# Kernel tuning notes

Hardware: AMD Instinct MI355X
Metric: run time of the kernel (lower is better)

The kernel has to match this reference:

```python
import jax, jax.numpy as jnp
import numpy as np

S, N, F, E, H = 64, 1000, 64, 128, 2  # seq_len, nodes/graph, node_dim, emb_dim, heads
DEG = 8
C = E // H  # per-head channels


def setup_inputs() -> dict:
    key = jax.random.key(0)
    ks = jax.random.split(key, 16)
    Ntot = S * N
    Eg = N * DEG
    src = jax.random.randint(ks[0], (S, Eg), 0, N)
    dst = jax.random.randint(ks[1], (S, Eg), 0, N)
    off = (jnp.arange(S) * N)[:, None]
    edge_index = jnp.stack([(src + off).reshape(-1), (dst + off).reshape(-1)]).astype(jnp.int32)
    nfm = jax.random.normal(ks[2], (Ntot, F), jnp.float32)
    reachable = jax.random.uniform(ks[3], (S, N)) > 0.2
    reachable = reachable.at[:, 0].set(True)  # ensure each row has a reachable node
    h0 = jnp.zeros((N, E), jnp.float32)
    c0 = jnp.zeros((N, E), jnp.float32)

    def lin(k, i, o):
        return (jax.random.normal(k, (i, o), jnp.float32) / np.sqrt(i)).astype(jnp.float32)

    return dict(
        nfm=nfm, edge_index=edge_index, reachable=reachable, h0=h0, c0=c0,
        gat_W1=lin(ks[4], F, E), gat_b1=jnp.zeros((E,), jnp.float32),
        gat_att1=(jax.random.normal(ks[5], (H, C), jnp.float32) / np.sqrt(C)).astype(jnp.float32),
        gat_bias1=jnp.zeros((E,), jnp.float32),
        gat_W=(jax.random.normal(ks[6], (4, E, E), jnp.float32) / np.sqrt(E)).astype(jnp.float32),
        gat_b=jnp.zeros((4, E), jnp.float32),
        gat_att=(jax.random.normal(ks[7], (4, H, C), jnp.float32) / np.sqrt(C)).astype(jnp.float32),
        gat_bias=jnp.zeros((4, E), jnp.float32),
        lstm_Wih=(jax.random.normal(ks[8], (4 * E, E), jnp.float32) / np.sqrt(E)).astype(jnp.float32),
        lstm_Whh=(jax.random.normal(ks[9], (4 * E, E), jnp.float32) / np.sqrt(E)).astype(jnp.float32),
        lstm_bih=jnp.zeros((4 * E,), jnp.float32), lstm_bhh=jnp.zeros((4 * E,), jnp.float32),
        th6_W=lin(ks[10], E, E), th6_b=jnp.zeros((E,), jnp.float32),
        th7_W=lin(ks[11], E, E), th7_b=jnp.zeros((E,), jnp.float32),
        th5_W=lin(ks[12], 2 * E, 1), th5_b=jnp.zeros((1,), jnp.float32),
    )


def _gat_layer(x, src, dst, W, b, att, bias, Ntot):
    # GATv2Conv, share_weights=True: x_l == x_r = lin(x)
    Hh, Ch = att.shape
    xl = (x @ W + b).reshape(-1, Hh, Ch)                 # [Ntot,H,C]
    e = jax.nn.leaky_relu(xl[src] + xl[dst], 0.2)        # [Etot,H,C]
    logit = jnp.einsum('ehc,hc->eh', e, att)             # [Etot,H]
    m = jax.ops.segment_max(logit, dst, num_segments=Ntot)
    a = jnp.exp(logit - m[dst])                          # segment-stable softmax
    denom = jax.ops.segment_sum(a, dst, num_segments=Ntot)
    alpha = a / denom[dst]
    out = jax.ops.segment_sum(xl[src] * alpha[:, :, None], dst, num_segments=Ntot)
    return out.reshape(-1, Hh * Ch) + bias               # concat heads + bias


def _forward(nfm, edge_index, reachable, h0, c0, gat_W1, gat_b1, gat_att1, gat_bias1,
             gat_W, gat_b, gat_att, gat_bias, lstm_Wih, lstm_Whh, lstm_bih, lstm_bhh,
             th6_W, th6_b, th7_W, th7_b, th5_W, th5_b):
    Ntot = nfm.shape[0]
    loops = jnp.arange(Ntot, dtype=edge_index.dtype)     # add_self_loops=True
    src = jnp.concatenate([edge_index[0], loops])
    dst = jnp.concatenate([edge_index[1], loops])

    x = jax.nn.relu(_gat_layer(nfm, src, dst, gat_W1, gat_b1, gat_att1, gat_bias1, Ntot))
    for i in range(4):  # layers 2..5; no activation after last
        x = _gat_layer(x, src, dst, gat_W[i], gat_b[i], gat_att[i], gat_bias[i], Ntot)
        if i < 3:
            x = jax.nn.relu(x)

    mu = x.reshape(S, N, E)                              # [seq, batch(=nodes), emb]

    def step(carry, xt):
        h, c = carry
        g = xt @ lstm_Wih.T + lstm_bih + h @ lstm_Whh.T + lstm_bhh
        i_, f_, gg, o_ = jnp.split(g, 4, axis=-1)        # torch gate order i,f,g,o
        c = jax.nn.sigmoid(f_) * c + jax.nn.sigmoid(i_) * jnp.tanh(gg)
        h = jax.nn.sigmoid(o_) * jnp.tanh(c)
        return (h, c), h

    (hT, cT), mu = jax.lax.scan(step, (h0, c0), mu)      # mu: [S,N,E]

    meanpool = mu.mean(axis=1, keepdims=True)            # [S,1,E]
    gs = meanpool @ th6_W + th6_b
    la = mu @ th7_W + th7_b
    rep = jax.nn.relu(jnp.concatenate([jnp.broadcast_to(gs, la.shape), la], axis=-1))
    logits = (rep @ th5_W)[..., 0] + th5_b               # [S,N]
    logits = jnp.where(reachable, logits, -jnp.inf)
    prob = jax.nn.softmax(logits, axis=1)
    return prob, hT, cT


def reference(nfm, edge_index, reachable, h0, c0, gat_W1, gat_b1, gat_att1, gat_bias1,
              gat_W, gat_b, gat_att, gat_bias, lstm_Wih, lstm_Whh, lstm_bih, lstm_bhh,
              th6_W, th6_b, th7_W, th7_b, th5_W, th5_b):
    return _forward(nfm, edge_index, reachable, h0, c0, gat_W1, gat_b1, gat_att1, gat_bias1,
                    gat_W, gat_b, gat_att, gat_bias, lstm_Wih, lstm_Whh, lstm_bih, lstm_bhh,
                    th6_W, th6_b, th7_W, th7_b, th5_W, th5_b)
```

## Files before the change

### kernel.cpp

```cpp
#include <hip/hip_runtime.h>
#include <hip/hip_bf16.h>

#define SQ   64
#define NN   1000
#define NT   64000
#define EE   128
#define EG   512000
#define ET   576000

#define WS_XA      0ull
#define WS_XB      33000000ull
#define WS_ROWPTR  66000000ull
#define WS_CURSOR  66300000ull
#define WS_SRCS    66600000ull
#define WS_INCL    69000000ull
#define WS_BSUM    69300000ull
#define WS_BOFF    69302048ull
#define WS_MODE    69304096ull
#define WS_WQA     70000000ull
#define WS_WQB     70262144ull
#define WS_AS      70600000ull
#define WS_LOGIT2  70700000ull
#define WS2_XC     33000000ull
#define WS2_BFRAG  164100000ull
#define WS2_GHI    164300000ull
#define WS2_GLO    164650000ull
#define WS2_B512   165000000ull
#define WS2_MODE   165010000ull
#define WS2_AS     165020000ull
#define WS2_LOGIT2 165100000ull
#define WS2_NEED   165360000ull
#define G_W1    0
#define G_WL    8192
#define G_PROJ  73728
#define G_W7    139264

typedef __attribute__((ext_vector_type(8))) short short8;
typedef __attribute__((ext_vector_type(4))) float f32x4;

__device__ __forceinline__ float rdlane(float v, int l) {
    return __int_as_float(__builtin_amdgcn_readlane(__float_as_int(v), l));
}
__device__ __forceinline__ float sigm(float x) { return 1.0f / (1.0f + __expf(-x)); }
__device__ __forceinline__ float tanh_f(float x) {
    x = fminf(fmaxf(x, -30.0f), 30.0f);
    float e = __expf(2.0f * x);
    return (e - 1.0f) / (e + 1.0f);
}
__device__ __forceinline__ float tanh2(float x) {
    return 2.0f / (1.0f + __expf(-2.0f * x)) - 1.0f;
}
__device__ __forceinline__ ushort f2bf(float x) {
    unsigned u = __float_as_uint(x);
    unsigned r = (u + 0x7FFFu + ((u >> 16) & 1u)) >> 16;
    return (ushort)r;
}
__device__ __forceinline__ float bf2f(ushort h) {
    return __uint_as_float(((unsigned)h) << 16);
}

__global__ void detect_mode_k(const unsigned char* __restrict__ p, int* __restrict__ mode) {
    __shared__ int f0, f3;
    const int t = threadIdx.x;
    if (t == 0) { f0 = 0; f3 = 0; }
    __syncthreads();
    int l0 = 0, l3 = 0;
    for (int i = t; i < 16000; i += 256) {
        if (p[4 * i])     l0 = 1;
        if (p[4 * i + 3]) l3 = 1;
    }
    if (l0) atomicOr(&f0, 1);
    if (l3) atomicOr(&f3, 1);
    __syncthreads();
    if (t == 0) {
        int m;
        if (f0 && f3)      m = 1;
        else if (f0)       m = 0;
        else               m = 2;
        *mode = m;
    }
}

__global__ void zero_ints_k(int* __restrict__ p, int n) {
    int i = blockIdx.x * 256 + threadIdx.x;
    if (i < n) p[i] = 0;
}
__global__ void hist_k(const int* __restrict__ ei, int* __restrict__ deg) {
    int e = blockIdx.x * 256 + threadIdx.x;
    if (e < ET) {
        int d = (e < EG) ? ei[EG + e] : (e - EG);
        atomicAdd(deg + d, 1);
    }
}
__global__ void scan1_k(const int* __restrict__ deg, int* __restrict__ incl, int* __restrict__ bsum) {
    __shared__ int sh[256];
    const int t = threadIdx.x;
    const int i = blockIdx.x * 256 + t;
    sh[t] = deg[i];
    __syncthreads();
    for (int o = 1; o < 256; o <<= 1) {
        int add = (t >= o) ? sh[t - o] : 0;
        __syncthreads();
        sh[t] += add;
        __syncthreads();
    }
    incl[i] = sh[t];
    if (t == 255) bsum[blockIdx.x] = sh[255];
}
__global__ void scan2_k(const int* __restrict__ bsum, int* __restrict__ boff) {
    __shared__ int sh[256];
    const int t = threadIdx.x;
    int v = (t < 250) ? bsum[t] : 0;
    sh[t] = v;
    __syncthreads();
    for (int o = 1; o < 256; o <<= 1) {
        int add = (t >= o) ? sh[t - o] : 0;
        __syncthreads();
        sh[t] += add;
        __syncthreads();
    }
    if (t < 250) boff[t] = sh[t] - v;
}
__global__ void scan3_k(const int* __restrict__ incl, const int* __restrict__ boff,
                        int* __restrict__ rowptr, int* __restrict__ cursor_deg) {
    const int i = blockIdx.x * 256 + threadIdx.x;
    int total = incl[i] + boff[blockIdx.x];
    int excl  = total - cursor_deg[i];
    rowptr[i] = excl;
    cursor_deg[i] = excl;
    if (i == NT - 1) rowptr[NT] = total;
}
__global__ void fill_k(const int* __restrict__ ei, int* __restrict__ cursor, int* __restrict__ srcs) {
    int e = blockIdx.x * 256 + threadIdx.x;
    if (e < ET) {
        int s_, d_;
        if (e < EG) { s_ = ei[e]; d_ = ei[EG + e]; }
        else        { s_ = e - EG; d_ = s_; }
        int p = atomicAdd(cursor + d_, 1);
        srcs[p] = s_;
    }
}

__global__ void build_gfrag_k(const float* __restrict__ src, const int ks, const int ns,
                              const int K, ushort* __restrict__ dhi, ushort* __restrict__ dlo,
                              const int total) {
    int id = blockIdx.x * 256 + threadIdx.x;
    if (id < total) {
        int j = id & 7, lane = (id >> 3) & 63;
        int f = id >> 9;
        int KT = K >> 5;
        int nt = f / KT, kt = f - nt * KT;
        int n = nt * 16 + (lane & 15);
        int k = kt * 32 + ((lane >> 4) << 3) + j;
        float v = src[(size_t)k * ks + (size_t)n * ns];
        ushort h = f2bf(v);
        dhi[id] = h;
        dlo[id] = f2bf(v - bf2f(h));
    }
}
__global__ void bias512_k(const float* __restrict__ bih, const float* __restrict__ bhh,
                          float* __restrict__ b512) {
    int i = blockIdx.x * 256 + threadIdx.x;
    if (i < 512) b512[i] = bih[i] + bhh[i];
}

template <int KT>
__global__ __launch_bounds__(256) void gemm_mf(
    const float* __restrict__ x, const ushort* __restrict__ bhi,
    const ushort* __restrict__ blo, const float* __restrict__ bias,
    float* __restrict__ out, const int ldout)
{
    constexpr int K = KT * 32;
    __shared__ __align__(16) ushort ahi_s[KT * 4 * 64 * 8];
    __shared__ __align__(16) ushort alo_s[KT * 4 * 64 * 8];
    const int t = threadIdx.x;
    const int w = t >> 6, lane = t & 63;
    const int quad = lane >> 4, col = lane & 15;
    const int row0 = blockIdx.x * 64;
    const int col0 = blockIdx.y * 128;

    {
        const int r  = t >> 2;
        const int kc = (t & 3) * (K / 4);
        const int rw = r >> 4, rcol = r & 15;
        const float* xr = x + (size_t)(row0 + r) * K + kc;
#pragma unroll
        for (int k = 0; k < K / 4; k += 4) {
            const int ch = kc + k;
            const int idx = (((ch >> 5) * 4 + rw) * 64 + ((ch >> 3) & 3) * 16 + rcol) * 8
                            + (ch & 7);
            float4 v = *(const float4*)(xr + k);
            ushort h0_ = f2bf(v.x), h1_ = f2bf(v.y), h2_ = f2bf(v.z), h3_ = f2bf(v.w);
            ushort l0_ = f2bf(v.x - bf2f(h0_)), l1_ = f2bf(v.y - bf2f(h1_));
            ushort l2_ = f2bf(v.z - bf2f(h2_)), l3_ = f2bf(v.w - bf2f(h3_));
            *(uint2*)(ahi_s + idx) = make_uint2((uint)h0_ | ((uint)h1_ << 16),
                                                (uint)h2_ | ((uint)h3_ << 16));
            *(uint2*)(alo_s + idx) = make_uint2((uint)l0_ | ((uint)l1_ << 16),
                                                (uint)l2_ | ((uint)l3_ << 16));
        }
    }
    __syncthreads();

    short8 ah[KT], al[KT];
#pragma unroll
    for (int kt = 0; kt < KT; kt++) {
        const int off = ((kt * 4 + w) * 64 + lane) * 8;
        ah[kt] = *(const short8*)(ahi_s + off);
        al[kt] = *(const short8*)(alo_s + off);
    }

    f32x4 acc[8];
#pragma unroll
    for (int q = 0; q < 8; q++) acc[q] = (f32x4){0.f, 0.f, 0.f, 0.f};

#pragma unroll
    for (int q = 0; q < 8; q++) {
#pragma unroll
        for (int kt = 0; kt < KT; kt++) {
            const int f = ((((col0 >> 4) + q) * KT + kt) * 64 + lane) * 8;
            short8 bh = *(const short8*)(bhi + f);
            short8 bl = *(const short8*)(blo + f);
            acc[q] = __builtin_amdgcn_mfma_f32_16x16x32_bf16(ah[kt], bh, acc[q], 0, 0, 0);
            acc[q] = __builtin_amdgcn_mfma_f32_16x16x32_bf16(al[kt], bh, acc[q], 0, 0, 0);
            acc[q] = __builtin_amdgcn_mfma_f32_16x16x32_bf16(ah[kt], bl, acc[q], 0, 0, 0);
        }
    }

#pragma unroll
    for (int q = 0; q < 8; q++) {
        float bv = bias[col0 + q * 16 + col];
#pragma unroll
        for (int r = 0; r < 4; r++) {
            out[(size_t)(row0 + w * 16 + quad * 4 + r) * ldout + col0 + q * 16 + col]
                = acc[q][r] + bv;
        }
    }
}

template <int K>
__global__ __launch_bounds__(256) void gemm3(
    const float* __restrict__ x, const float* __restrict__ W,
    const float* __restrict__ b, float* __restrict__ out)
{
    __shared__ float Wsh[64 * 128];
    __shared__ float xT[64][132];
    const int t = threadIdx.x;
    const int row0 = blockIdx.x * 128;
    const int cg = t & 15;
    const int rg = t >> 4;
    float4 acc[8][2];
#pragma unroll
    for (int r = 0; r < 8; r++) {
        acc[r][0] = make_float4(0.f, 0.f, 0.f, 0.f);
        acc[r][1] = make_float4(0.f, 0.f, 0.f, 0.f);
    }
    for (int k0 = 0; k0 < K; k0 += 64) {
        for (int i = t * 4; i < 64 * 128; i += 1024)
            *(float4*)(Wsh + i) = *(const float4*)(W + (size_t)k0 * 128 + i);
        for (int i = t * 4; i < 128 * 64; i += 1024) {
            int r = i >> 6, k = i & 63;
            float4 v = *(const float4*)(x + (size_t)(row0 + r) * K + k0 + k);
            xT[k + 0][r] = v.x; xT[k + 1][r] = v.y;
            xT[k + 2][r] = v.z; xT[k + 3][r] = v.w;
        }
        __syncthreads();
#pragma unroll 2
        for (int k = 0; k < 64; k++) {
            float4 w0 = *(const float4*)(Wsh + k * 128 + cg * 8);
            float4 w1 = *(const float4*)(Wsh + k * 128 + cg * 8 + 4);
            float4 x0 = *(const float4*)(&xT[k][rg * 8]);
            float4 x1 = *(const float4*)(&xT[k][rg * 8 + 4]);
            float xv[8] = {x0.x, x0.y, x0.z, x0.w, x1.x, x1.y, x1.z, x1.w};
#pragma unroll
            for (int r = 0; r < 8; r++) {
                acc[r][0].x += xv[r] * w0.x; acc[r][0].y += xv[r] * w0.y;
                acc[r][0].z += xv[r] * w0.z; acc[r][0].w += xv[r] * w0.w;
                acc[r][1].x += xv[r] * w1.x; acc[r][1].y += xv[r] * w1.y;
                acc[r][1].z += xv[r] * w1.z; acc[r][1].w += xv[r] * w1.w;
            }
        }
        __syncthreads();
    }
    float4 bv0 = *(const float4*)(b + cg * 8);
    float4 bv1 = *(const float4*)(b + cg * 8 + 4);
#pragma unroll
    for (int r = 0; r < 8; r++) {
        float4 o0, o1;
        o0.x = acc[r][0].x + bv0.x; o0.y = acc[r][0].y + bv0.y;
        o0.z = acc[r][0].z + bv0.z; o0.w = acc[r][0].w + bv0.w;
        o1.x = acc[r][1].x + bv1.x; o1.y = acc[r][1].y + bv1.y;
        o1.z = acc[r][1].z + bv1.z; o1.w = acc[r][1].w + bv1.w;
        float* op = out + (size_t)(row0 + rg * 8 + r) * 128 + cg * 8;
        *(float4*)(op) = o0;
        *(float4*)(op + 4) = o1;
    }
}

__global__ __launch_bounds__(256) void gat_fused_k(
    const float* __restrict__ xl, const int* __restrict__ rowptr,
    const int* __restrict__ srcs, const float* __restrict__ att,
    const float* __restrict__ bias, float* __restrict__ out, const int do_relu)
{
    const int lane = threadIdx.x & 63;
    const int q = lane & 31;
    const int h = lane >> 5;
    const int b = blockIdx.x;
    const int g = b & 7;
    const int j = b >> 3;
    const int jq = j / 250;
    const int jj = j - jq * 250;
    const int s = g + 8 * jq;
    const int n = s * NN + jj * 4 + (threadIdx.x >> 6);

    const float4 a4 = *(const float4*)(att + q * 4);
    const float4 xd = *(const float4*)(xl + (size_t)n * 128 + q * 4);
    const int i0 = rowptr[n], i1 = rowptr[n + 1];

    float m = -1e30f, d = 0.f;
    float ax = 0.f, ay = 0.f, az = 0.f, aw = 0.f;

    int i = i0 + h;
    int sv = (i < i1) ? srcs[i] : 0;
    for (int base = i0; base < i1; base += 2) {
        const bool valid = (i < i1);
        const int svn = (i + 2 < i1) ? srcs[i + 2] : 0;
        const float4 xs = *(const float4*)(xl + (size_t)sv * 128 + q * 4);
        float u0 = xs.x + xd.x, u1 = xs.y + xd.y;
        float u2 = xs.z + xd.z, u3 = xs.w + xd.w;
        float p;
        p  = a4.x * fmaxf(u0, 0.2f * u0);
        p += a4.y * fmaxf(u1, 0.2f * u1);
        p += a4.z * fmaxf(u2, 0.2f * u2);
        p += a4.w * fmaxf(u3, 0.2f * u3);
        p += __shfl_xor(p, 1);
        p += __shfl_xor(p, 2);
        p += __shfl_xor(p, 4);
        p += __shfl_xor(p, 8);
        float mn = fmaxf(m, valid ? p : -1e30f);
        float sc = __expf(m - mn);
        float wgt = valid ? __expf(p - mn) : 0.f;
        d  = d  * sc + wgt;
        ax = ax * sc + wgt * xs.x;
        ay = ay * sc + wgt * xs.y;
        az = az * sc + wgt * xs.z;
        aw = aw * sc + wgt * xs.w;
        m = mn;
        sv = svn;
        i += 2;
    }

    float m2 = __shfl_xor(m, 32);
    float d2 = __shfl_xor(d, 32);
    float bx = __shfl_xor(ax, 32);
    float by = __shfl_xor(ay, 32);
    float bz = __shfl_xor(az, 32);
    float bw = __shfl_xor(aw, 32);
    float mm = fmaxf(m, m2);
    float s1 = __expf(m - mm), s2 = __expf(m2 - mm);
    float den = d * s1 + d2 * s2;
    float inv = 1.f / den;
    float4 bv = *(const float4*)(bias + q * 4);
    float ox = (ax * s1 + bx * s2) * inv + bv.x;
    float oy = (ay * s1 + by * s2) * inv + bv.y;
    float oz = (az * s1 + bz * s2) * inv + bv.z;
    float ow = (aw * s1 + bw * s2) * inv + bv.w;
    if (do_relu) {
        ox = fmaxf(ox, 0.f); oy = fmaxf(oy, 0.f);
        oz = fmaxf(oz, 0.f); ow = fmaxf(ow, 0.f);
    }
    if (lane < 32)
        *(float4*)(out + (size_t)n * 128 + q * 4) = make_float4(ox, oy, oz, ow);
}

__global__ void build_wq_k(const float* __restrict__ Wih, const float* __restrict__ Whh,
                           float4* __restrict__ WQa, float4* __restrict__ WQb) {
    int id = blockIdx.x * 256 + threadIdx.x;
    if (id < 64 * 256) {
        int kp = id >> 8, t = id & 255;
        int j1 = t, j2 = t + 256;
        WQa[id] = make_float4(Wih[(size_t)j1 * 128 + 2 * kp], Whh[(size_t)j1 * 128 + 2 * kp],
                              Wih[(size_t)j1 * 128 + 2 * kp + 1], Whh[(size_t)j1 * 128 + 2 * kp + 1]);
        WQb[id] = make_float4(Wih[(size_t)j2 * 128 + 2 * kp], Whh[(size_t)j2 * 128 + 2 * kp],
                              Wih[(size_t)j2 * 128 + 2 * kp + 1], Whh[(size_t)j2 * 128 + 2 * kp + 1]);
    }
}

__global__ void build_bfrag_k(const float* __restrict__ Whh, ushort* __restrict__ Bfrag) {
    int id = blockIdx.x * 256 + threadIdx.x;
    if (id < 65536) {
        int j = id & 7, lane = (id >> 3) & 63, kt = (id >> 9) & 3, tile = id >> 11;
        int gate = tile * 16 + (lane & 15);
        int k = kt * 32 + ((lane >> 4) << 3) + j;
        Bfrag[id] = f2bf(Whh[(size_t)gate * 128 + k]);
    }
}

#define LSTM_GROUP(buf, gbase)                                                     \
    _Pragma("unroll")                                                              \
    for (int i_ = 0; i_ < 4; i_++) {                                               \
        const int kp_ = (gbase) * 4 + i_;                                          \
        const float4 qa_ = buf[i_];                                                \
        const float4 qb_ = buf[4 + i_];                                            \
        _Pragma("unroll")                                                          \
        for (int n_ = 0; n_ < 4; n_++) {                                           \
            const float sx0_ = rdlane(xr[n_].x, kp_);                              \
            const float sh0_ = rdlane(hr[n_].x, kp_);                              \
            const float sx1_ = rdlane(xr[n_].y, kp_);                              \
            const float sh1_ = rdlane(hr[n_].y, kp_);                              \
            acc1[n_] += sx0_ * qa_.x + sh0_ * qa_.y + sx1_ * qa_.z + sh1_ * qa_.w; \
            acc2[n_] += sx0_ * qb_.x + sh0_ * qb_.y + sx1_ * qb_.z + sh1_ * qb_.w; \
        }                                                                          \
    }

__global__ __launch_bounds__(256, 1) void lstm_k(
    float* __restrict__ mu, const float4* __restrict__ WQa, const float4* __restrict__ WQb,
    const float* __restrict__ bih, const float* __restrict__ bhh,
    const float* __restrict__ h0, const float* __restrict__ c0,
    float* __restrict__ hT, float* __restrict__ cT)
{
    const int t = threadIdx.x, lane = t & 63;
    const int n0 = blockIdx.x * 4;
    __shared__ float hsh[4][128];
    __shared__ float gsh[4][512];
    const float b1 = bih[t] + bhh[t];
    const float b2 = bih[t + 256] + bhh[t + 256];
    float creg[2];
#pragma unroll
    for (int q = 0; q < 2; q++) {
        int id = t + 256 * q;
        creg[q] = c0[(size_t)(n0 + (id >> 7)) * 128 + (id & 127)];
    }
    for (int i = t; i < 512; i += 256)
        hsh[i >> 7][i & 127] = h0[(size_t)(n0 + (i >> 7)) * 128 + (i & 127)];

    const float4* pA = WQa + t;
    const float4* pB = WQb + t;

    float2 xr[4], xnx[4];
#pragma unroll
    for (int n = 0; n < 4; n++)
        xr[n] = *(const float2*)(mu + (size_t)n0 * 128 + n * 128 + lane * 2);
    __syncthreads();

    for (int s = 0; s < SQ; s++) {
        float* xrow = mu + ((size_t)s * NN + n0) * 128;
        float2 hr[4];
#pragma unroll
        for (int n = 0; n < 4; n++) hr[n] = *(const float2*)(&hsh[n][lane * 2]);

        float4 bufA[8], bufB[8];
#pragma unroll
        for (int i = 0; i < 4; i++) { bufA[i] = pA[i * 256]; bufA[4 + i] = pB[i * 256]; }

        if (s + 1 < SQ) {
            const float* xrow2 = mu + ((size_t)(s + 1) * NN + n0) * 128;
#pragma unroll
            for (int n = 0; n < 4; n++) xnx[n] = *(const float2*)(xrow2 + n * 128 + lane * 2);
        }

        float acc1[4], acc2[4];
#pragma unroll
        for (int n = 0; n < 4; n++) { acc1[n] = b1; acc2[n] = b2; }

        for (int g = 0; g < 16; g += 2) {
#pragma unroll
            for (int i = 0; i < 4; i++) {
                bufB[i]     = pA[((g + 1) * 4 + i) * 256];
                bufB[4 + i] = pB[((g + 1) * 4 + i) * 256];
            }
            LSTM_GROUP(bufA, g)
            if (g < 14) {
#pragma unroll
                for (int i = 0; i < 4; i++) {
                    bufA[i]     = pA[((g + 2) * 4 + i) * 256];
                    bufA[4 + i] = pB[((g + 2) * 4 + i) * 256];
                }
            }
            LSTM_GROUP(bufB, g + 1)
        }

#pragma unroll
        for (int n = 0; n < 4; n++) { gsh[n][t] = acc1[n]; gsh[n][t + 256] = acc2[n]; }
        __syncthreads();
#pragma unroll
        for (int q = 0; q < 2; q++) {
            int id = t + 256 * q;
            int n = id >> 7, e = id & 127;
            float iv = gsh[n][e], fv = gsh[n][128 + e];
            float gv = gsh[n][256 + e], ov = gsh[n][384 + e];
            float c = sigm(fv) * creg[q] + sigm(iv) * tanh_f(gv);
            float h = sigm(ov) * tanh_f(c);
            creg[q] = c;
            hsh[n][e] = h;
            xrow[n * 128 + e] = h;
            if (s == SQ - 1) {
                hT[(size_t)(n0 + n) * 128 + e] = h;
                cT[(size_t)(n0 + n) * 128 + e] = c;
            }
        }
#pragma unroll
        for (int n = 0; n < 4; n++) xr[n] = xnx[n];
        __syncthreads();
    }
}

__global__ __launch_bounds__(512, 2) void lstm10_k(
    float* __restrict__ mu, const float* __restrict__ xC,
    const ushort* __restrict__ Bfrag,
    const float* __restrict__ h0, const float* __restrict__ c0,
    float* __restrict__ hT, float* __restrict__ cT)
{
    const int t = threadIdx.x;
    const int w = t >> 6, lane = t & 63;
    const int quad = lane >> 4;
    const int n0 = blockIdx.x * 4;
    const int enode = t >> 7;
    const int ech   = t & 127;

    __shared__ __align__(16) ushort hP[2][2][2048];
    __shared__ float gsh[4][512];

    short8 bf[4][4];
#pragma unroll
    for (int g4 = 0; g4 < 4; g4++)
#pragma unroll
        for (int kt = 0; kt < 4; kt++) {
            int tile = g4 * 8 + w;
            bf[g4][kt] = *(const short8*)(Bfrag + (((tile * 4 + kt) * 64 + lane) << 3));
        }

    const int epkt = ech >> 5, epqd = (ech >> 3) & 3, epj = ech & 7;
    const int epidx = epkt * 512 + (epqd * 16 + enode) * 8 + epj;

    for (int i = t; i < 2 * 2 * 2048; i += 512) ((ushort*)hP)[i] = 0;
    __syncthreads();
    {
        float v = h0[(size_t)(n0 + enode) * 128 + ech];
        ushort hh = f2bf(v), hl = f2bf(v - bf2f(hh));
        hP[0][0][epidx] = hh; hP[0][1][epidx] = hl;
        hP[1][0][epidx] = hh; hP[1][1][epidx] = hl;
    }
    float cst = c0[(size_t)(n0 + enode) * 128 + ech];

    float xcr[4], xcn[4];
#pragma unroll
    for (int g4 = 0; g4 < 4; g4++)
        xcr[g4] = xC[((size_t)(n0 + enode)) * 512 + g4 * 128 + ech];
    __syncthreads();

    int p = 0;
    for (int s = 0; s < SQ; s++) {
        if (s + 1 < SQ) {
            const float* xn = xC + ((size_t)(s + 1) * NN + n0 + enode) * 512;
#pragma unroll
            for (int g4 = 0; g4 < 4; g4++)
                xcn[g4] = xn[g4 * 128 + ech];
        }

        short8 ahi[4], alo[4];
#pragma unroll
        for (int kt = 0; kt < 4; kt++) {
            ahi[kt] = *(const short8*)(&hP[p][0][kt * 512 + lane * 8]);
            alo[kt] = *(const short8*)(&hP[p][1][kt * 512 + lane * 8]);
        }

        f32x4 acc[4];
#pragma unroll
        for (int g4 = 0; g4 < 4; g4++) acc[g4] = (f32x4){0.f, 0.f, 0.f, 0.f};
#pragma unroll
        for (int kt = 0; kt < 4; kt++) {
#pragma unroll
            for (int g4 = 0; g4 < 4; g4++)
                acc[g4] = __builtin_amdgcn_mfma_f32_16x16x32_bf16(ahi[kt], bf[g4][kt], acc[g4], 0, 0, 0);
#pragma unroll
            for (int g4 = 0; g4 < 4; g4++)
                acc[g4] = __builtin_amdgcn_mfma_f32_16x16x32_bf16(alo[kt], bf[g4][kt], acc[g4], 0, 0, 0);
        }

        if (quad == 0) {
            const int col = lane & 15;
#pragma unroll
            for (int g4 = 0; g4 < 4; g4++)
#pragma unroll
                for (int r = 0; r < 4; r++)
                    gsh[r][(g4 * 8 + w) * 16 + col] = acc[g4][r];
        }
        __syncthreads();

        {
            float iv = gsh[enode][0 * 128 + ech] + xcr[0];
            float fv = gsh[enode][1 * 128 + ech] + xcr[1];
            float gv = gsh[enode][2 * 128 + ech] + xcr[2];
            float ov = gsh[enode][3 * 128 + ech] + xcr[3];
            float c = sigm(fv) * cst + sigm(iv) * tanh2(gv);
            float h = sigm(ov) * tanh2(c);
            cst = c;
            const int pn = p ^ 1;
            ushort hh = f2bf(h);
            hP[pn][0][epidx] = hh;
            hP[pn][1][epidx] = f2bf(h - bf2f(hh));
            mu[((size_t)s * NN + n0 + enode) * 128 + ech] = h;
            if (s == SQ - 1) {
                hT[(size_t)(n0 + enode) * 128 + ech] = h;
                cT[(size_t)(n0 + enode) * 128 + ech] = c;
            }
            p = pn;
        }
#pragma unroll
        for (int g4 = 0; g4 < 4; g4++) xcr[g4] = xcn[g4];
        __syncthreads();
    }
}

__global__ __launch_bounds__(256) void meanpool_gs_k(
    const float* __restrict__ mu, const float* __restrict__ W6,
    const float* __restrict__ b6, const float* __restrict__ w5,
    float* __restrict__ A)
{
    const int s = blockIdx.x, t = threadIdx.x;
    const int ch = t & 127, half = t >> 7;
    __shared__ float mp[128];
    __shared__ float red[256];
    float acc = 0.f;
    for (int n = half * 500; n < (half + 1) * 500; n++)
        acc += mu[((size_t)s * NN + n) * 128 + ch];
    red[t] = acc;
    __syncthreads();
    if (t < 128) mp[t] = (red[t] + red[t + 128]) * 0.001f;
    __syncthreads();
    float g = 0.f;
    if (t < 128) {
        g = b6[t];
        for (int k = 0; k < 128; k++) g += mp[k] * W6[(size_t)k * 128 + t];
        g = fmaxf(g, 0.f) * w5[t];
    }
    red[t] = g;
    __syncthreads();
    for (int o = 128; o > 0; o >>= 1) {
        if (t < o) red[t] += red[t + o];
        __syncthreads();
    }
    if (t == 0) A[s] = red[0];
}

__global__ __launch_bounds__(256) void rowdot_k(
    const float* __restrict__ la, const float* __restrict__ w5,
    const float* __restrict__ b5, const float* __restrict__ A,
    float* __restrict__ out)
{
    const int lane = threadIdx.x & 63;
    const int row = blockIdx.x * 4 + (threadIdx.x >> 6);
    float2 v = *(const float2*)(la + (size_t)row * 128 + lane * 2);
    float2 w = *(const float2*)(w5 + 128 + lane * 2);
    float x = fmaxf(v.x, 0.f) * w.x + fmaxf(v.y, 0.f) * w.y;
#pragma unroll
    for (int o = 32; o; o >>= 1) x += __shfl_down(x, o);
    if (lane == 0) out[row] = x + A[row / NN] + b5[0];
}

__device__ __forceinline__ bool reach_at(const void* reach, int mode, int idx) {
    if (mode == 0) return ((const int*)reach)[idx] != 0;
    if (mode == 1) return ((const unsigned char*)reach)[idx] != 0;
    return ((const float*)reach)[idx] != 0.f;
}
__global__ __launch_bounds__(256) void softmax_k(
    const float* __restrict__ lg, const void* __restrict__ reach,
    const int* __restrict__ mode, float* __restrict__ prob)
{
    const int s = blockIdx.x, t = threadIdx.x;
    const int m = *mode;
    __shared__ float red[256];
    float mx = -1e30f;
    for (int i = t; i < NN; i += 256) {
        int idx = s * NN + i;
        if (reach_at(reach, m, idx)) mx = fmaxf(mx, lg[idx]);
    }
    red[t] = mx;
    __syncthreads();
    for (int o = 128; o; o >>= 1) {
        if (t < o) red[t] = fmaxf(red[t], red[t + o]);
        __syncthreads();
    }
    mx = red[0];
    __syncthreads();
    float sum = 0.f;
    for (int i = t; i < NN; i += 256) {
        int idx = s * NN + i;
        float v = reach_at(reach, m, idx) ? __expf(lg[idx] - mx) : 0.f;
        prob[idx] = v;
        sum += v;
    }
    red[t] = sum;
    __syncthreads();
    for (int o = 128; o; o >>= 1) {
        if (t < o) red[t] += red[t + o];
        __syncthreads();
    }
    float inv = 1.f / red[0];
    for (int i = t; i < NN; i += 256) prob[s * NN + i] *= inv;
}

extern "C" void kernel_launch(void* const* d_in, const int* in_sizes, int n_in,
                              void* d_out, int out_size, void* d_ws, size_t ws_size,
                              hipStream_t stream) {
    const float* nfm   = (const float*)d_in[0];
    const int*   ei    = (const int*)d_in[1];
    const void*  reach = d_in[2];
    const float* h0    = (const float*)d_in[3];
    const float* c0    = (const float*)d_in[4];
    const float* W1    = (const float*)d_in[5];
    const float* b1    = (const float*)d_in[6];
    const float* att1  = (const float*)d_in[7];
    const float* bias1 = (const float*)d_in[8];
    const float* Wl    = (const float*)d_in[9];
    const float* bl    = (const float*)d_in[10];
    const float* attl  = (const float*)d_in[11];
    const float* biasl = (const float*)d_in[12];
    const float* Wih   = (const float*)d_in[13];
    const float* Whh   = (const float*)d_in[14];
    const float* bih   = (const float*)d_in[15];
    const float* bhh   = (const float*)d_in[16];
    const float* W6    = (const float*)d_in[17];
    const float* b6    = (const float*)d_in[18];
    const float* W7    = (const float*)d_in[19];
    const float* b7    = (const float*)d_in[20];
    const float* w5    = (const float*)d_in[21];
    const float* b5    = (const float*)d_in[22];

    char* ws = (char*)d_ws;
    const bool bigws = (ws_size >= WS2_NEED);

    float*  xA     = (float*)(ws + WS_XA);
    float*  xB     = (float*)(ws + WS_XB);
    int*    rowptr = (int*)(ws + WS_ROWPTR);
    int*    cursor = (int*)(ws + WS_CURSOR);
    int*    srcs   = (int*)(ws + WS_SRCS);
    int*    incl   = (int*)(ws + WS_INCL);
    int*    bsum   = (int*)(ws + WS_BSUM);
    int*    boff   = (int*)(ws + WS_BOFF);
    int*    modep  = bigws ? (int*)(ws + WS2_MODE)     : (int*)(ws + WS_MODE);
    float*  As     = bigws ? (float*)(ws + WS2_AS)     : (float*)(ws + WS_AS);
    float*  logit2 = bigws ? (float*)(ws + WS2_LOGIT2) : (float*)(ws + WS_LOGIT2);
    float*  xC     = (float*)(ws + WS2_XC);
    ushort* Bfrag  = (ushort*)(ws + WS2_BFRAG);
    ushort* ghi    = (ushort*)(ws + WS2_GHI);
    ushort* glo    = (ushort*)(ws + WS2_GLO);
    float*  b512   = (float*)(ws + WS2_B512);
    float4* WQa    = (float4*)(ws + WS_WQA);
    float4* WQb    = (float4*)(ws + WS_WQB);

    float* prob = (float*)d_out;
    float* hT   = (float*)d_out + 64000;
    float* cT   = (float*)d_out + 192000;

    detect_mode_k<<<1, 256, 0, stream>>>((const unsigned char*)reach, modep);
    zero_ints_k<<<250, 256, 0, stream>>>(cursor, NT);
    hist_k<<<2250, 256, 0, stream>>>(ei, cursor);
    scan1_k<<<250, 256, 0, stream>>>(cursor, incl, bsum);
    scan2_k<<<1, 256, 0, stream>>>(bsum, boff);
    scan3_k<<<250, 256, 0, stream>>>(incl, boff, rowptr, cursor);
    fill_k<<<2250, 256, 0, stream>>>(ei, cursor, srcs);
    if (bigws) {
        build_bfrag_k<<<256, 256, 0, stream>>>(Whh, Bfrag);
        bias512_k<<<2, 256, 0, stream>>>(bih, bhh, b512);
        build_gfrag_k<<<32, 256, 0, stream>>>(W1, 128, 1, 64, ghi + G_W1, glo + G_W1, 8192);
        for (int i = 0; i < 4; i++)
            build_gfrag_k<<<64, 256, 0, stream>>>(Wl + (size_t)i * 16384, 128, 1, 128,
                                                  ghi + G_WL + i * 16384, glo + G_WL + i * 16384, 16384);
        build_gfrag_k<<<256, 256, 0, stream>>>(Wih, 1, 128, 128, ghi + G_PROJ, glo + G_PROJ, 65536);
        build_gfrag_k<<<64, 256, 0, stream>>>(W7, 128, 1, 128, ghi + G_W7, glo + G_W7, 16384);
    } else {
        build_wq_k<<<64, 256, 0, stream>>>(Wih, Whh, WQa, WQb);
    }

    for (int l = 0; l < 5; l++) {
        if (bigws) {
            if (l == 0)
                gemm_mf<2><<<dim3(1000, 1), 256, 0, stream>>>(nfm, ghi + G_W1, glo + G_W1, b1, xB, 128);
            else
                gemm_mf<4><<<dim3(1000, 1), 256, 0, stream>>>(xA, ghi + G_WL + (l - 1) * 16384,
                                                              glo + G_WL + (l - 1) * 16384,
                                                              bl + (l - 1) * 128, xB, 128);
        } else {
            if (l == 0)
                gemm3<64><<<500, 256, 0, stream>>>(nfm, W1, b1, xB);
            else
                gemm3<128><<<500, 256, 0, stream>>>(xA, Wl + (size_t)(l - 1) * 128 * 128,
                                                    bl + (l - 1) * 128, xB);
        }
        const float* att  = (l == 0) ? att1  : attl  + (l - 1) * 128;
        const float* bias = (l == 0) ? bias1 : biasl + (l - 1) * 128;
        gat_fused_k<<<16000, 256, 0, stream>>>(xB, rowptr, srcs, att, bias, xA,
                                               (l < 4) ? 1 : 0);
    }

    if (bigws) {
        gemm_mf<4><<<dim3(1000, 4), 256, 0, stream>>>(xA, ghi + G_PROJ, glo + G_PROJ, b512, xC, 512);
        lstm10_k<<<250, 512, 0, stream>>>(xA, xC, Bfrag, h0, c0, hT, cT);
    } else {
        lstm_k<<<250, 256, 0, stream>>>(xA, WQa, WQb, bih, bhh, h0, c0, hT, cT);
    }

    meanpool_gs_k<<<64, 256, 0, stream>>>(xA, W6, b6, w5, As);
    if (bigws)
        gemm_mf<4><<<dim3(1000, 1), 256, 0, stream>>>(xA, ghi + G_W7, glo + G_W7, b7, xB, 128);
    else
        gemm3<128><<<500, 256, 0, stream>>>(xA, W7, b7, xB);
    rowdot_k<<<16000, 256, 0, stream>>>(xB, w5, b5, As, logit2);
    softmax_k<<<64, 256, 0, stream>>>(logit2, reach, modep, prob);
}
```

Baseline: 692.9 us.

## Split LSTM recurrence across 16 waves and deepen GAT gather prefetch

The LSTM recurrence kernel now runs 1024 threads per block, so each of 16 waves computes two MFMA gate tiles per step instead of eight waves computing four. This shortens the serial per-step MFMA chain on the critical path. The upper 512 threads only take part in the matmul and barriers, and the elementwise epilogue stays on the first 512. Separately, the GAT aggregation loop now prefetches neighbour feature rows two iterations ahead rather than loading them in the current one, to hide gather latency at the cost of extra registers.

```diff
diff --git a/kernel.cpp b/kernel.cpp
--- a/kernel.cpp
+++ b/kernel.cpp
@@ -320,13 +320,17 @@
     float ax = 0.f, ay = 0.f, az = 0.f, aw = 0.f;
 
     int i = i0 + h;
-    int sv = (i < i1) ? srcs[i] : 0;
+    int sv0 = (i < i1) ? srcs[i] : 0;
+    int sv1 = (i + 2 < i1) ? srcs[i + 2] : 0;
+    float4 xs0 = *(const float4*)(xl + (size_t)sv0 * 128 + q * 4);
+    float4 xs1 = *(const float4*)(xl + (size_t)sv1 * 128 + q * 4);
+
     for (int base = i0; base < i1; base += 2) {
         const bool valid = (i < i1);
-        const int svn = (i + 2 < i1) ? srcs[i + 2] : 0;
-        const float4 xs = *(const float4*)(xl + (size_t)sv * 128 + q * 4);
-        float u0 = xs.x + xd.x, u1 = xs.y + xd.y;
-        float u2 = xs.z + xd.z, u3 = xs.w + xd.w;
+        const int svn = (i + 4 < i1) ? srcs[i + 4] : 0;
+        const float4 xsn = *(const float4*)(xl + (size_t)svn * 128 + q * 4);
+        float u0 = xs0.x + xd.x, u1 = xs0.y + xd.y;
+        float u2 = xs0.z + xd.z, u3 = xs0.w + xd.w;
         float p;
         p  = a4.x * fmaxf(u0, 0.2f * u0);
         p += a4.y * fmaxf(u1, 0.2f * u1);
@@ -340,12 +344,12 @@
         float sc = __expf(m - mn);
         float wgt = valid ? __expf(p - mn) : 0.f;
         d  = d  * sc + wgt;
-        ax = ax * sc + wgt * xs.x;
-        ay = ay * sc + wgt * xs.y;
-        az = az * sc + wgt * xs.z;
-        aw = aw * sc + wgt * xs.w;
+        ax = ax * sc + wgt * xs0.x;
+        ay = ay * sc + wgt * xs0.y;
+        az = az * sc + wgt * xs0.z;
+        aw = aw * sc + wgt * xs0.w;
         m = mn;
-        sv = svn;
+        xs0 = xs1; xs1 = xsn;
         i += 2;
     }
 
@@ -504,7 +508,7 @@
     }
 }
 
-__global__ __launch_bounds__(512, 2) void lstm10_k(
+__global__ __launch_bounds__(1024, 4) void lstm11_k(
     float* __restrict__ mu, const float* __restrict__ xC,
     const ushort* __restrict__ Bfrag,
     const float* __restrict__ h0, const float* __restrict__ c0,
@@ -514,43 +518,44 @@
     const int w = t >> 6, lane = t & 63;
     const int quad = lane >> 4;
     const int n0 = blockIdx.x * 4;
-    const int enode = t >> 7;
+    const int enode = (t >> 7) & 3;
     const int ech   = t & 127;
+    const bool epi  = (t < 512);
 
     __shared__ __align__(16) ushort hP[2][2][2048];
     __shared__ float gsh[4][512];
 
-    short8 bf[4][4];
-#pragma unroll
-    for (int g4 = 0; g4 < 4; g4++)
+    short8 bf[2][4];
+#pragma unroll
+    for (int g2 = 0; g2 < 2; g2++)
 #pragma unroll
         for (int kt = 0; kt < 4; kt++) {
-            int tile = g4 * 8 + w;
-            bf[g4][kt] = *(const short8*)(Bfrag + (((tile * 4 + kt) * 64 + lane) << 3));
+            int tile = g2 * 16 + w;
+            bf[g2][kt] = *(const short8*)(Bfrag + (((tile * 4 + kt) * 64 + lane) << 3));
         }
 
     const int epkt = ech >> 5, epqd = (ech >> 3) & 3, epj = ech & 7;
     const int epidx = epkt * 512 + (epqd * 16 + enode) * 8 + epj;
 
-    for (int i = t; i < 2 * 2 * 2048; i += 512) ((ushort*)hP)[i] = 0;
-    __syncthreads();
-    {
+    for (int i = t; i < 2 * 2 * 2048; i += 1024) ((ushort*)hP)[i] = 0;
+    __syncthreads();
+    float cst = 0.f;
+    float xcr[4], xcn[4];
+    if (epi) {
         float v = h0[(size_t)(n0 + enode) * 128 + ech];
         ushort hh = f2bf(v), hl = f2bf(v - bf2f(hh));
         hP[0][0][epidx] = hh; hP[0][1][epidx] = hl;
         hP[1][0][epidx] = hh; hP[1][1][epidx] = hl;
-    }
-    float cst = c0[(size_t)(n0 + enode) * 128 + ech];
-
-    float xcr[4], xcn[4];
-#pragma unroll
-    for (int g4 = 0; g4 < 4; g4++)
-        xcr[g4] = xC[((size_t)(n0 + enode)) * 512 + g4 * 128 + ech];
+        cst = c0[(size_t)(n0 + enode) * 128 + ech];
+#pragma unroll
+        for (int g4 = 0; g4 < 4; g4++)
+            xcr[g4] = xC[((size_t)(n0 + enode)) * 512 + g4 * 128 + ech];
+    }
     __syncthreads();
 
     int p = 0;
     for (int s = 0; s < SQ; s++) {
-        if (s + 1 < SQ) {
+        if (epi && s + 1 < SQ) {
             const float* xn = xC + ((size_t)(s + 1) * NN + n0 + enode) * 512;
 #pragma unroll
             for (int g4 = 0; g4 < 4; g4++)
@@ -564,30 +569,30 @@
             alo[kt] = *(const short8*)(&hP[p][1][kt * 512 + lane * 8]);
         }
 
-        f32x4 acc[4];
-#pragma unroll
-        for (int g4 = 0; g4 < 4; g4++) acc[g4] = (f32x4){0.f, 0.f, 0.f, 0.f};
+        f32x4 acc[2];
+#pragma unroll
+        for (int g2 = 0; g2 < 2; g2++) acc[g2] = (f32x4){0.f, 0.f, 0.f, 0.f};
 #pragma unroll
         for (int kt = 0; kt < 4; kt++) {
 #pragma unroll
-            for (int g4 = 0; g4 < 4; g4++)
-                acc[g4] = __builtin_amdgcn_mfma_f32_16x16x32_bf16(ahi[kt], bf[g4][kt], acc[g4], 0, 0, 0);
-#pragma unroll
-            for (int g4 = 0; g4 < 4; g4++)
-                acc[g4] = __builtin_amdgcn_mfma_f32_16x16x32_bf16(alo[kt], bf[g4][kt], acc[g4], 0, 0, 0);
+            for (int g2 = 0; g2 < 2; g2++)
+                acc[g2] = __builtin_amdgcn_mfma_f32_16x16x32_bf16(ahi[kt], bf[g2][kt], acc[g2], 0, 0, 0);
+#pragma unroll
+            for (int g2 = 0; g2 < 2; g2++)
+                acc[g2] = __builtin_amdgcn_mfma_f32_16x16x32_bf16(alo[kt], bf[g2][kt], acc[g2], 0, 0, 0);
         }
 
         if (quad == 0) {
             const int col = lane & 15;
 #pragma unroll
-            for (int g4 = 0; g4 < 4; g4++)
+            for (int g2 = 0; g2 < 2; g2++)
 #pragma unroll
                 for (int r = 0; r < 4; r++)
-                    gsh[r][(g4 * 8 + w) * 16 + col] = acc[g4][r];
-        }
-        __syncthreads();
-
-        {
+                    gsh[r][g2 * 256 + w * 16 + col] = acc[g2][r];
+        }
+        __syncthreads();
+
+        if (epi) {
             float iv = gsh[enode][0 * 128 + ech] + xcr[0];
             float fv = gsh[enode][1 * 128 + ech] + xcr[1];
             float gv = gsh[enode][2 * 128 + ech] + xcr[2];
@@ -604,10 +609,10 @@
                 hT[(size_t)(n0 + enode) * 128 + ech] = h;
                 cT[(size_t)(n0 + enode) * 128 + ech] = c;
             }
-            p = pn;
-        }
-#pragma unroll
-        for (int g4 = 0; g4 < 4; g4++) xcr[g4] = xcn[g4];
+#pragma unroll
+            for (int g4 = 0; g4 < 4; g4++) xcr[g4] = xcn[g4];
+        }
+        p ^= 1;
         __syncthreads();
     }
 }
@@ -796,7 +801,7 @@
 
     if (bigws) {
         gemm_mf<4><<<dim3(1000, 4), 256, 0, stream>>>(xA, ghi + G_PROJ, glo + G_PROJ, b512, xC, 512);
-        lstm10_k<<<250, 512, 0, stream>>>(xA, xC, Bfrag, h0, c0, hT, cT);
+        lstm11_k<<<250, 1024, 0, stream>>>(xA, xC, Bfrag, h0, c0, hT, cT);
     } else {
         lstm_k<<<250, 256, 0, stream>>>(xA, WQa, WQb, bih, bhh, h0, c0, hT, cT);
     }
```

Result: no change. 690.6 us (-0.3%).

## Apply LSTM gates in MFMA registers and deepen GAT gather prefetch

Applied to the files above, without the earlier changes.

The LSTM step now has the quad-0 lanes, which hold the MFMA accumulators for all four gates of a node, compute the gate nonlinearities straight from registers. This removes the shared-memory gate staging buffer and one block barrier per timestep. In exchange only a quarter of the lanes do the elementwise work, and their mu stores are less coalesced. Separately, the GAT aggregation loop prefetches neighbor feature rows two iterations ahead instead of only prefetching the index, to hide gather latency at the cost of extra registers.

```diff
diff --git a/kernel.cpp b/kernel.cpp
--- a/kernel.cpp
+++ b/kernel.cpp
@@ -320,13 +320,17 @@
     float ax = 0.f, ay = 0.f, az = 0.f, aw = 0.f;
 
     int i = i0 + h;
-    int sv = (i < i1) ? srcs[i] : 0;
+    int sv0 = (i < i1) ? srcs[i] : 0;
+    int sv1 = (i + 2 < i1) ? srcs[i + 2] : 0;
+    float4 xs0 = *(const float4*)(xl + (size_t)sv0 * 128 + q * 4);
+    float4 xs1 = *(const float4*)(xl + (size_t)sv1 * 128 + q * 4);
+
     for (int base = i0; base < i1; base += 2) {
         const bool valid = (i < i1);
-        const int svn = (i + 2 < i1) ? srcs[i + 2] : 0;
-        const float4 xs = *(const float4*)(xl + (size_t)sv * 128 + q * 4);
-        float u0 = xs.x + xd.x, u1 = xs.y + xd.y;
-        float u2 = xs.z + xd.z, u3 = xs.w + xd.w;
+        const int svn = (i + 4 < i1) ? srcs[i + 4] : 0;
+        const float4 xsn = *(const float4*)(xl + (size_t)svn * 128 + q * 4);
+        float u0 = xs0.x + xd.x, u1 = xs0.y + xd.y;
+        float u2 = xs0.z + xd.z, u3 = xs0.w + xd.w;
         float p;
         p  = a4.x * fmaxf(u0, 0.2f * u0);
         p += a4.y * fmaxf(u1, 0.2f * u1);
@@ -340,12 +344,12 @@
         float sc = __expf(m - mn);
         float wgt = valid ? __expf(p - mn) : 0.f;
         d  = d  * sc + wgt;
-        ax = ax * sc + wgt * xs.x;
-        ay = ay * sc + wgt * xs.y;
-        az = az * sc + wgt * xs.z;
-        aw = aw * sc + wgt * xs.w;
+        ax = ax * sc + wgt * xs0.x;
+        ay = ay * sc + wgt * xs0.y;
+        az = az * sc + wgt * xs0.z;
+        aw = aw * sc + wgt * xs0.w;
         m = mn;
-        sv = svn;
+        xs0 = xs1; xs1 = xsn;
         i += 2;
     }
 
@@ -504,7 +508,7 @@
     }
 }
 
-__global__ __launch_bounds__(512, 2) void lstm10_k(
+__global__ __launch_bounds__(512, 2) void lstm12_k(
     float* __restrict__ mu, const float* __restrict__ xC,
     const ushort* __restrict__ Bfrag,
     const float* __restrict__ h0, const float* __restrict__ c0,
@@ -512,13 +516,11 @@
 {
     const int t = threadIdx.x;
     const int w = t >> 6, lane = t & 63;
-    const int quad = lane >> 4;
+    const int quad = lane >> 4, col = lane & 15;
     const int n0 = blockIdx.x * 4;
-    const int enode = t >> 7;
-    const int ech   = t & 127;
+    const int e = w * 16 + col;
 
     __shared__ __align__(16) ushort hP[2][2][2048];
-    __shared__ float gsh[4][512];
 
     short8 bf[4][4];
 #pragma unroll
@@ -529,32 +531,37 @@
             bf[g4][kt] = *(const short8*)(Bfrag + (((tile * 4 + kt) * 64 + lane) << 3));
         }
 
-    const int epkt = ech >> 5, epqd = (ech >> 3) & 3, epj = ech & 7;
-    const int epidx = epkt * 512 + (epqd * 16 + enode) * 8 + epj;
+    const int ebase = (e >> 5) * 512 + (((e >> 3) & 3) * 16) * 8 + (e & 7);
 
     for (int i = t; i < 2 * 2 * 2048; i += 512) ((ushort*)hP)[i] = 0;
     __syncthreads();
-    {
-        float v = h0[(size_t)(n0 + enode) * 128 + ech];
-        ushort hh = f2bf(v), hl = f2bf(v - bf2f(hh));
-        hP[0][0][epidx] = hh; hP[0][1][epidx] = hl;
-        hP[1][0][epidx] = hh; hP[1][1][epidx] = hl;
-    }
-    float cst = c0[(size_t)(n0 + enode) * 128 + ech];
-
-    float xcr[4], xcn[4];
-#pragma unroll
-    for (int g4 = 0; g4 < 4; g4++)
-        xcr[g4] = xC[((size_t)(n0 + enode)) * 512 + g4 * 128 + ech];
+
+    float cst[4];
+    float xcr[4][4], xcn[4][4];
+    if (quad == 0) {
+#pragma unroll
+        for (int r = 0; r < 4; r++) {
+            float v = h0[(size_t)(n0 + r) * 128 + e];
+            ushort hh = f2bf(v), hl = f2bf(v - bf2f(hh));
+            hP[0][0][ebase + r * 8] = hh; hP[0][1][ebase + r * 8] = hl;
+            hP[1][0][ebase + r * 8] = hh; hP[1][1][ebase + r * 8] = hl;
+            cst[r] = c0[(size_t)(n0 + r) * 128 + e];
+#pragma unroll
+            for (int g4 = 0; g4 < 4; g4++)
+                xcr[g4][r] = xC[(size_t)(n0 + r) * 512 + g4 * 128 + e];
+        }
+    }
     __syncthreads();
 
     int p = 0;
     for (int s = 0; s < SQ; s++) {
-        if (s + 1 < SQ) {
-            const float* xn = xC + ((size_t)(s + 1) * NN + n0 + enode) * 512;
-#pragma unroll
-            for (int g4 = 0; g4 < 4; g4++)
-                xcn[g4] = xn[g4 * 128 + ech];
+        if (quad == 0 && s + 1 < SQ) {
+            const float* xn = xC + ((size_t)(s + 1) * NN + n0) * 512;
+#pragma unroll
+            for (int r = 0; r < 4; r++)
+#pragma unroll
+                for (int g4 = 0; g4 < 4; g4++)
+                    xcn[g4][r] = xn[(size_t)r * 512 + g4 * 128 + e];
         }
 
         short8 ahi[4], alo[4];
@@ -577,37 +584,31 @@
                 acc[g4] = __builtin_amdgcn_mfma_f32_16x16x32_bf16(alo[kt], bf[g4][kt], acc[g4], 0, 0, 0);
         }
 
+        const int pn = p ^ 1;
         if (quad == 0) {
-            const int col = lane & 15;
-#pragma unroll
-            for (int g4 = 0; g4 < 4; g4++)
-#pragma unroll
-                for (int r = 0; r < 4; r++)
-                    gsh[r][(g4 * 8 + w) * 16 + col] = acc[g4][r];
-        }
-        __syncthreads();
-
-        {
-            float iv = gsh[enode][0 * 128 + ech] + xcr[0];
-            float fv = gsh[enode][1 * 128 + ech] + xcr[1];
-            float gv = gsh[enode][2 * 128 + ech] + xcr[2];
-            float ov = gsh[enode][3 * 128 + ech] + xcr[3];
-            float c = sigm(fv) * cst + sigm(iv) * tanh2(gv);
-            float h = sigm(ov) * tanh2(c);
-            cst = c;
-            const int pn = p ^ 1;
-            ushort hh = f2bf(h);
-            hP[pn][0][epidx] = hh;
-            hP[pn][1][epidx] = f2bf(h - bf2f(hh));
-            mu[((size_t)s * NN + n0 + enode) * 128 + ech] = h;
-            if (s == SQ - 1) {
-                hT[(size_t)(n0 + enode) * 128 + ech] = h;
-                cT[(size_t)(n0 + enode) * 128 + ech] = c;
+            float* mus = mu + (size_t)s * (NN * 128);
+#pragma unroll
+            for (int r = 0; r < 4; r++) {
+                float iv = acc[0][r] + xcr[0][r];
+                float fv = acc[1][r] + xcr[1][r];
+                float gv = acc[2][r] + xcr[2][r];
+                float ov = acc[3][r] + xcr[3][r];
+                float c = sigm(fv) * cst[r] + sigm(iv) * tanh2(gv);
+                float h = sigm(ov) * tanh2(c);
+                cst[r] = c;
+                ushort hh = f2bf(h);
+                hP[pn][0][ebase + r * 8] = hh;
+                hP[pn][1][ebase + r * 8] = f2bf(h - bf2f(hh));
+                mus[(size_t)(n0 + r) * 128 + e] = h;
+                if (s == SQ - 1) {
+                    hT[(size_t)(n0 + r) * 128 + e] = h;
+                    cT[(size_t)(n0 + r) * 128 + e] = c;
+                }
+#pragma unroll
+                for (int g4 = 0; g4 < 4; g4++) xcr[g4][r] = xcn[g4][r];
             }
-            p = pn;
-        }
-#pragma unroll
-        for (int g4 = 0; g4 < 4; g4++) xcr[g4] = xcn[g4];
+        }
+        p = pn;
         __syncthreads();
     }
 }
@@ -796,7 +797,7 @@
 
     if (bigws) {
         gemm_mf<4><<<dim3(1000, 4), 256, 0, stream>>>(xA, ghi + G_PROJ, glo + G_PROJ, b512, xC, 512);
-        lstm10_k<<<250, 512, 0, stream>>>(xA, xC, Bfrag, h0, c0, hT, cT);
+        lstm12_k<<<250, 512, 0, stream>>>(xA, xC, Bfrag, h0, c0, hT, cT);
     } else {
         lstm_k<<<250, 256, 0, stream>>>(xA, WQa, WQb, bih, bhh, h0, c0, hT, cT);
     }
```

After: 755.2 us. 9.0% more time.
